# Performance work log

Measured on AMD Instinct MI355X. Metric: run time of the kernel, lower is better.

The kernel has to match this reference:

```python
import jax, jax.numpy as jnp
import numpy as np

B, M, L, IN_C, MID_C, OUT_C = 1, 128, 256, 256, 32, 128


def setup_inputs() -> dict:
    key = jax.random.key(0)
    k_x, k_proj, k_final = jax.random.split(key, 3)
    return {
        "x1d": jax.random.normal(k_x, (B, M, L, IN_C), dtype=jnp.float32),
        "norm_w": jnp.ones((IN_C,), dtype=jnp.float32),
        "norm_b": jnp.zeros((IN_C,), dtype=jnp.float32),
        "proj_w": jax.random.normal(k_proj, (2 * MID_C, IN_C), dtype=jnp.float32) * 0.02,
        "proj_b": jnp.zeros((2 * MID_C,), dtype=jnp.float32),
        "final_w": jax.random.normal(k_final, (OUT_C, MID_C * MID_C), dtype=jnp.float32) * 0.02,
        "final_b": jnp.zeros((OUT_C,), dtype=jnp.float32),
    }


def reference(x1d, norm_w, norm_b, proj_w, proj_b, final_w, final_b):
    # LayerNorm over channel dim
    mu = jnp.mean(x1d, axis=-1, keepdims=True)
    var = jnp.mean(jnp.square(x1d - mu), axis=-1, keepdims=True)
    x = (x1d - mu) * jax.lax.rsqrt(var + 1e-5) * norm_w + norm_b

    mid_c = proj_w.shape[0] // 2
    # Linear -> (b, m, L, 2*mid_c); view (..., mid_c, 2); chunk & squeeze:
    # i = interleaved even channels, j = interleaved odd channels
    p = jnp.einsum('bmlc,dc->bmld', x, proj_w) + proj_b
    p = p.reshape(*p.shape[:-1], mid_c, 2)
    i, j = p[..., 0], p[..., 1]          # each (b, m, L, mid_c)

    m = x1d.shape[1]
    # Outer product mean over the MSA (m) dimension -> (b, L, L, mid_c, mid_c)
    x2d = jnp.einsum('bmix,bmjy->bijxy', i, j) / m

    b, li, lj = x2d.shape[0], x2d.shape[1], x2d.shape[2]
    flat = x2d.reshape(b, li, lj, mid_c * mid_c)
    out = jnp.einsum('bijf,of->bijo', flat, final_w) + final_b
    return out
```

## Files before the change

kernel.cpp:

```cpp
#include <hip/hip_runtime.h>
#include <hip/hip_bf16.h>

#define DEVINL __device__ __forceinline__

typedef float  f32x4_t  __attribute__((ext_vector_type(4)));
typedef float  f32x16_t __attribute__((ext_vector_type(16)));
typedef short  bf16x8_t __attribute__((ext_vector_type(8)));

#define MFMA16(a,b,c) __builtin_amdgcn_mfma_f32_16x16x32_bf16((a),(b),(c),0,0,0)
#define MFMA32(a,b,c) __builtin_amdgcn_mfma_f32_32x32x16_bf16((a),(b),(c),0,0,0)

DEVINL unsigned short f2bf(float f) {
  union { float f; unsigned u; } v; v.f = f;
  unsigned r = v.u + 0x7fffu + ((v.u >> 16) & 1u);
  return (unsigned short)(r >> 16);
}

DEVINL unsigned pk2bf(float lo, float hi) {
  union { __hip_bfloat162 h2; unsigned u; } v;
  v.h2 = __float22bfloat162_rn(make_float2(lo, hi));
  return v.u;
}


__global__ __launch_bounds__(256) void kA(const float* __restrict__ x,
                                          const float* __restrict__ nw,
                                          const float* __restrict__ nb,
                                          const float* __restrict__ pw,
                                          const float* __restrict__ pb,
                                          const float* __restrict__ fw,
                                          unsigned short* __restrict__ Wb,
                                          unsigned short* __restrict__ Ig,
                                          unsigned short* __restrict__ Jg) {
  if (blockIdx.x >= 1024) {
    int T = (blockIdx.x - 1024) * 256 + threadIdx.x;
    int o     = T >> 8;
    int kpos0 = (T & 255) * 4;
    int y  = kpos0 >> 5;
    int x0 = kpos0 & 31;
    const float* fo = fw + o * 1024 + y;
    ushort4 u;
    u.x = f2bf(fo[(x0 + 0) * 32]);
    u.y = f2bf(fo[(x0 + 1) * 32]);
    u.z = f2bf(fo[(x0 + 2) * 32]);
    u.w = f2bf(fo[(x0 + 3) * 32]);
    size_t off = (size_t)((o >> 5) * 64 + (kpos0 >> 4)) * 512 + (o & 31) * 16
               + ((kpos0 >> 3) & 1) * 8 + (kpos0 & 7);
    *(ushort4*)&Wb[off] = u;
    return;
  }
  __shared__ unsigned short xnl[32 * 264];
  __shared__ unsigned short pwl[64 * 264];
  __shared__ unsigned short ep[64 * 36];
  const int tid  = threadIdx.x;
  const int wv   = tid >> 6;
  const int lane = tid & 63;
  const int q    = lane >> 4;
  const int ln16 = lane & 15;
  const int l    = blockIdx.x & 255;
  const int m0   = (blockIdx.x >> 8) * 32;

  const float4* xs = (const float4*)x;
  float4 v[8];
#pragma unroll
  for (int i = 0; i < 8; i++) {
    int row = m0 + i * 4 + wv;
    v[i] = xs[row * 16384 + l * 64 + lane];
  }
  float4 nw4 = ((const float4*)nw)[lane];
  float4 nb4 = ((const float4*)nb)[lane];

#pragma unroll
  for (int i = 0; i < 8; i++) {
    float s  = v[i].x + v[i].y + v[i].z + v[i].w;
    float ss = v[i].x * v[i].x + v[i].y * v[i].y + v[i].z * v[i].z + v[i].w * v[i].w;
#pragma unroll
    for (int off = 32; off > 0; off >>= 1) {
      s  += __shfl_xor(s, off);
      ss += __shfl_xor(ss, off);
    }
    float mu  = s * (1.0f / 256.0f);
    float var = ss * (1.0f / 256.0f) - mu * mu;
    float rs  = rsqrtf(var + 1e-5f);
    ushort4 u;
    u.x = f2bf((v[i].x - mu) * rs * nw4.x + nb4.x);
    u.y = f2bf((v[i].y - mu) * rs * nw4.y + nb4.y);
    u.z = f2bf((v[i].z - mu) * rs * nw4.z + nb4.z);
    u.w = f2bf((v[i].w - mu) * rs * nw4.w + nb4.w);
    *(ushort4*)&xnl[(i * 4 + wv) * 264 + lane * 4] = u;
  }

  const float4* ps = (const float4*)pw;
#pragma unroll
  for (int i = 0; i < 16; i++) {
    float4 w4 = ps[i * 256 + tid];
    ushort4 u;
    u.x = f2bf(w4.x); u.y = f2bf(w4.y); u.z = f2bf(w4.z); u.w = f2bf(w4.w);
    *(ushort4*)&pwl[(i * 4 + wv) * 264 + lane * 4] = u;
  }
  __syncthreads();

  const int rt = wv & 1;
  const int db = (wv >> 1) * 32;
  f32x4_t acc[2] = {{0.f, 0.f, 0.f, 0.f}, {0.f, 0.f, 0.f, 0.f}};
#pragma unroll
  for (int kc = 0; kc < 8; kc++) {
    bf16x8_t a  = *(const bf16x8_t*)&xnl[(rt * 16 + ln16) * 264 + kc * 32 + q * 8];
    bf16x8_t b0 = *(const bf16x8_t*)&pwl[(db + ln16) * 264 + kc * 32 + q * 8];
    bf16x8_t b1 = *(const bf16x8_t*)&pwl[(db + 16 + ln16) * 264 + kc * 32 + q * 8];
    acc[0] = MFMA16(a, b0, acc[0]);
    acc[1] = MFMA16(a, b1, acc[1]);
  }

#pragma unroll
  for (int t2 = 0; t2 < 2; t2++) {
    int d = db + t2 * 16 + ln16;
    float bias  = pb[d];
    float scale = (d & 1) ? 1.0f : (1.0f / 128.0f);
#pragma unroll
    for (int r = 0; r < 4; r++) {
      int mloc = rt * 16 + q * 4 + r;
      ep[d * 36 + mloc] = f2bf((acc[t2][r] + bias) * scale);
    }
  }
  __syncthreads();

  const int h  = tid >> 3;
  const int m4 = tid & 7;
  const size_t off = (size_t)(l * 8 + (m0 >> 4) + (m4 >> 2)) * 512 + h * 16 + ((m4 >> 1) & 1) * 8 + (m4 & 1) * 4;
  ushort4 vi = *(const ushort4*)&ep[(2 * h) * 36 + m4 * 4];
  *(ushort4*)&Ig[off] = vi;
  ushort4 vj = *(const ushort4*)&ep[(2 * h + 1) * 36 + m4 * 4];
  *(ushort4*)&Jg[off] = vj;
}

__global__ __launch_bounds__(256, 2) void kB(const unsigned short* __restrict__ Ig,
                                             const unsigned short* __restrict__ Jg,
                                             const unsigned short* __restrict__ Wb,
                                             const float* __restrict__ fb,
                                             float* __restrict__ out) {
  extern __shared__ unsigned short fl[];
  constexpr int P = 1048;
  const int tid  = threadIdx.x;
  const int w    = tid >> 6;
  const int lane = tid & 63;
  const int ln32 = lane & 31;
  const int h    = lane >> 5;
  const int p    = blockIdx.x >> 4;
  const int t    = blockIdx.x & 15;

  bf16x8_t af[2][8];
#pragma unroll
  for (int u = 0; u < 2; u++)
#pragma unroll
    for (int mc = 0; mc < 8; mc++)
      af[u][mc] = *(const bf16x8_t*)&Ig[(size_t)((p * 2 + u) * 8 + mc) * 512 + ln32 * 16 + h * 8];

#pragma unroll
  for (int s = 0; s < 4; s++) {
    const int jl = 4 * w + s;
    const size_t jbase = (size_t)(t * 16 + jl) * 4096 + ln32 * 16 + h * 8;
    bf16x8_t jb[8];
#pragma unroll
    for (int mc = 0; mc < 8; mc++) jb[mc] = *(const bf16x8_t*)&Jg[jbase + mc * 512];
    f32x16_t c[2];
#pragma unroll
    for (int i = 0; i < 16; i++) { c[0][i] = 0.f; c[1][i] = 0.f; }
#pragma unroll
    for (int mc = 0; mc < 8; mc++) {
      c[0] = MFMA32(af[0][mc], jb[mc], c[0]);
      c[1] = MFMA32(af[1][mc], jb[mc], c[1]);
    }
#pragma unroll
    for (int u = 0; u < 2; u++) {
      unsigned short* fr = &fl[(u * 16 + jl) * P];
#pragma unroll
      for (int g = 0; g < 4; g++) {
        int cp = (4 * ln32 + g) ^ (ln32 & 7);
        uint2 pv;
        pv.x = pk2bf(c[u][4 * g + 0], c[u][4 * g + 1]);
        pv.y = pk2bf(c[u][4 * g + 2], c[u][4 * g + 3]);
        *(uint2*)&fr[cp * 8 + h * 4] = pv;
      }
    }
  }

  const int ot = w;
  const unsigned short* Wp = Wb + (size_t)(ot * 64) * 512 + ln32 * 16 + h * 8;
  bf16x8_t bq[8];
  bq[0] = *(const bf16x8_t*)&Wp[0];
  bq[1] = *(const bf16x8_t*)&Wp[512];

  __syncthreads();

#pragma unroll
  for (int i = 2; i < 8; i++) bq[i] = *(const bf16x8_t*)&Wp[(size_t)i * 512];

#define LDA(kc) (*(const bf16x8_t*)&fl[ln32 * P + \
    (((((kc) * 2 + h)) ^ (((kc) >> 1) & 7)) * 8)])

  f32x16_t o2[2];
#pragma unroll
  for (int i = 0; i < 16; i++) { o2[0][i] = 0.f; o2[1][i] = 0.f; }

  bf16x8_t aq[4];
  aq[0] = LDA(0); aq[1] = LDA(1); aq[2] = LDA(2); aq[3] = LDA(3);

#pragma unroll
  for (int kc = 0; kc < 64; kc += 2) {
    bf16x8_t ac0 = aq[kc & 3],      ac1 = aq[(kc + 1) & 3];
    bf16x8_t bc0 = bq[kc & 7],      bc1 = bq[(kc + 1) & 7];
    if (kc < 60) { aq[kc & 3] = LDA(kc + 4); aq[(kc + 1) & 3] = LDA(kc + 5); }
    if (kc < 56) {
      bq[kc & 7]       = *(const bf16x8_t*)&Wp[(size_t)(kc + 8) * 512];
      bq[(kc + 1) & 7] = *(const bf16x8_t*)&Wp[(size_t)(kc + 9) * 512];
    }
    o2[0] = MFMA32(ac0, bc0, o2[0]);
    o2[1] = MFMA32(ac1, bc1, o2[1]);
  }
#undef LDA

  const float bias = fb[ot * 32 + ln32];
  float* ob = out + ((size_t)(p * 2) * 256 + t * 16) * 128 + ot * 32 + ln32;
#pragma unroll
  for (int r = 0; r < 16; r++) {
    int br = (r & 3) + 8 * (r >> 2) + 4 * h;
    ob[(br >> 4) * 32768 + (br & 15) * 128] = o2[0][r] + o2[1][r] + bias;
  }
}

extern "C" void kernel_launch(void* const* d_in, const int* in_sizes, int n_in,
                              void* d_out, int out_size, void* d_ws, size_t ws_size,
                              hipStream_t stream) {
  const float* x1d     = (const float*)d_in[0];
  const float* norm_w  = (const float*)d_in[1];
  const float* norm_b  = (const float*)d_in[2];
  const float* proj_w  = (const float*)d_in[3];
  const float* proj_b  = (const float*)d_in[4];
  const float* final_w = (const float*)d_in[5];
  const float* final_b = (const float*)d_in[6];
  float* outp          = (float*)d_out;

  unsigned short* Wb  = (unsigned short*)d_ws;
  unsigned short* Igp = Wb + 131072;
  unsigned short* Jgp = Igp + 1048576;

  const int kb_lds = 32 * 1048 * 2;
  hipFuncSetAttribute((const void*)kB, hipFuncAttributeMaxDynamicSharedMemorySize, kb_lds);

  kA<<<1152, 256, 0, stream>>>(x1d, norm_w, norm_b, proj_w, proj_b, final_w, Wb, Igp, Jgp);
  kB<<<2048, 256, kb_lds, stream>>>(Igp, Jgp, Wb, final_b, outp);
}
```

Baseline: 134.8 us.

## Double kB block to 512 threads with split-K final GEMM and LDS reduction

kB now launches 8 waves per block instead of 4. In the first stage each wave computes one of the two outer-product rows, and in the final projection each wave covers half of the K dimension for one output tile. The two K halves are summed through LDS before the bias-add store. This is meant to raise parallelism per block and cut per-wave register pressure, at the cost of an extra barrier and LDS reduction round. Occupancy is still capped by roughly 67KB of LDS per block.

```diff
diff --git a/kernel.cpp b/kernel.cpp
--- a/kernel.cpp
+++ b/kernel.cpp
@@ -134,7 +134,7 @@
   *(ushort4*)&Jg[off] = vj;
 }
 
-__global__ __launch_bounds__(256, 2) void kB(const unsigned short* __restrict__ Ig,
+__global__ __launch_bounds__(512, 4) void kB(const unsigned short* __restrict__ Ig,
                                              const unsigned short* __restrict__ Jg,
                                              const unsigned short* __restrict__ Wb,
                                              const float* __restrict__ fb,
@@ -149,44 +149,39 @@
   const int p    = blockIdx.x >> 4;
   const int t    = blockIdx.x & 15;
 
-  bf16x8_t af[2][8];
-#pragma unroll
-  for (int u = 0; u < 2; u++)
-#pragma unroll
-    for (int mc = 0; mc < 8; mc++)
-      af[u][mc] = *(const bf16x8_t*)&Ig[(size_t)((p * 2 + u) * 8 + mc) * 512 + ln32 * 16 + h * 8];
+  const int u  = w & 1;
+  const int sq = w >> 1;
+  bf16x8_t af[8];
+#pragma unroll
+  for (int mc = 0; mc < 8; mc++)
+    af[mc] = *(const bf16x8_t*)&Ig[(size_t)((p * 2 + u) * 8 + mc) * 512 + ln32 * 16 + h * 8];
 
 #pragma unroll
   for (int s = 0; s < 4; s++) {
-    const int jl = 4 * w + s;
+    const int jl = sq * 4 + s;
     const size_t jbase = (size_t)(t * 16 + jl) * 4096 + ln32 * 16 + h * 8;
     bf16x8_t jb[8];
 #pragma unroll
     for (int mc = 0; mc < 8; mc++) jb[mc] = *(const bf16x8_t*)&Jg[jbase + mc * 512];
-    f32x16_t c[2];
-#pragma unroll
-    for (int i = 0; i < 16; i++) { c[0][i] = 0.f; c[1][i] = 0.f; }
-#pragma unroll
-    for (int mc = 0; mc < 8; mc++) {
-      c[0] = MFMA32(af[0][mc], jb[mc], c[0]);
-      c[1] = MFMA32(af[1][mc], jb[mc], c[1]);
-    }
-#pragma unroll
-    for (int u = 0; u < 2; u++) {
-      unsigned short* fr = &fl[(u * 16 + jl) * P];
-#pragma unroll
-      for (int g = 0; g < 4; g++) {
-        int cp = (4 * ln32 + g) ^ (ln32 & 7);
-        uint2 pv;
-        pv.x = pk2bf(c[u][4 * g + 0], c[u][4 * g + 1]);
-        pv.y = pk2bf(c[u][4 * g + 2], c[u][4 * g + 3]);
-        *(uint2*)&fr[cp * 8 + h * 4] = pv;
-      }
-    }
-  }
-
-  const int ot = w;
-  const unsigned short* Wp = Wb + (size_t)(ot * 64) * 512 + ln32 * 16 + h * 8;
+    f32x16_t c;
+#pragma unroll
+    for (int i = 0; i < 16; i++) c[i] = 0.f;
+#pragma unroll
+    for (int mc = 0; mc < 8; mc++) c = MFMA32(af[mc], jb[mc], c);
+    unsigned short* fr = &fl[(u * 16 + jl) * P];
+#pragma unroll
+    for (int g = 0; g < 4; g++) {
+      int cp = (4 * ln32 + g) ^ (ln32 & 7);
+      uint2 pv;
+      pv.x = pk2bf(c[4 * g + 0], c[4 * g + 1]);
+      pv.y = pk2bf(c[4 * g + 2], c[4 * g + 3]);
+      *(uint2*)&fr[cp * 8 + h * 4] = pv;
+    }
+  }
+
+  const int ot = w & 3;
+  const int kh = w >> 2;
+  const unsigned short* Wp = Wb + (size_t)(ot * 64 + kh * 32) * 512 + ln32 * 16 + h * 8;
   bf16x8_t bq[8];
   bq[0] = *(const bf16x8_t*)&Wp[0];
   bq[1] = *(const bf16x8_t*)&Wp[512];
@@ -197,7 +192,7 @@
   for (int i = 2; i < 8; i++) bq[i] = *(const bf16x8_t*)&Wp[(size_t)i * 512];
 
 #define LDA(kc) (*(const bf16x8_t*)&fl[ln32 * P + \
-    (((((kc) * 2 + h)) ^ (((kc) >> 1) & 7)) * 8)])
+    ((((kh * 32 + (kc)) * 2 + h) ^ (((kh * 32 + (kc)) >> 1) & 7)) * 8)])
 
   f32x16_t o2[2];
 #pragma unroll
@@ -207,11 +202,11 @@
   aq[0] = LDA(0); aq[1] = LDA(1); aq[2] = LDA(2); aq[3] = LDA(3);
 
 #pragma unroll
-  for (int kc = 0; kc < 64; kc += 2) {
+  for (int kc = 0; kc < 32; kc += 2) {
     bf16x8_t ac0 = aq[kc & 3],      ac1 = aq[(kc + 1) & 3];
     bf16x8_t bc0 = bq[kc & 7],      bc1 = bq[(kc + 1) & 7];
-    if (kc < 60) { aq[kc & 3] = LDA(kc + 4); aq[(kc + 1) & 3] = LDA(kc + 5); }
-    if (kc < 56) {
+    if (kc < 28) { aq[kc & 3] = LDA(kc + 4); aq[(kc + 1) & 3] = LDA(kc + 5); }
+    if (kc < 24) {
       bq[kc & 7]       = *(const bf16x8_t*)&Wp[(size_t)(kc + 8) * 512];
       bq[(kc + 1) & 7] = *(const bf16x8_t*)&Wp[(size_t)(kc + 9) * 512];
     }
@@ -220,12 +215,35 @@
   }
 #undef LDA
 
-  const float bias = fb[ot * 32 + ln32];
-  float* ob = out + ((size_t)(p * 2) * 256 + t * 16) * 128 + ot * 32 + ln32;
-#pragma unroll
-  for (int r = 0; r < 16; r++) {
-    int br = (r & 3) + 8 * (r >> 2) + 4 * h;
-    ob[(br >> 4) * 32768 + (br & 15) * 128] = o2[0][r] + o2[1][r] + bias;
+#pragma unroll
+  for (int i = 0; i < 16; i++) o2[0][i] += o2[1][i];
+
+  __syncthreads();
+  float* red = (float*)fl;
+  if (kh == 1) {
+#pragma unroll
+    for (int q = 0; q < 4; q++) {
+      int idx = ot * 1024 + lane * 16 + ((q ^ (lane & 3)) * 4);
+      *(float4*)&red[idx] = make_float4(o2[0][4 * q + 0], o2[0][4 * q + 1],
+                                        o2[0][4 * q + 2], o2[0][4 * q + 3]);
+    }
+  }
+  __syncthreads();
+  if (kh == 0) {
+#pragma unroll
+    for (int q = 0; q < 4; q++) {
+      int idx = ot * 1024 + lane * 16 + ((q ^ (lane & 3)) * 4);
+      float4 rv = *(const float4*)&red[idx];
+      o2[0][4 * q + 0] += rv.x; o2[0][4 * q + 1] += rv.y;
+      o2[0][4 * q + 2] += rv.z; o2[0][4 * q + 3] += rv.w;
+    }
+    const float bias = fb[ot * 32 + ln32];
+    float* ob = out + ((size_t)(p * 2) * 256 + t * 16) * 128 + ot * 32 + ln32;
+#pragma unroll
+    for (int r = 0; r < 16; r++) {
+      int br = (r & 3) + 8 * (r >> 2) + 4 * h;
+      ob[(br >> 4) * 32768 + (br & 15) * 128] = o2[0][r] + bias;
+    }
   }
 }
 
@@ -249,5 +267,5 @@
   hipFuncSetAttribute((const void*)kB, hipFuncAttributeMaxDynamicSharedMemorySize, kb_lds);
 
   kA<<<1152, 256, 0, stream>>>(x1d, norm_w, norm_b, proj_w, proj_b, final_w, Wb, Igp, Jgp);
-  kB<<<2048, 256, kb_lds, stream>>>(Igp, Jgp, Wb, final_b, outp);
-}
+  kB<<<2048, 512, kb_lds, stream>>>(Igp, Jgp, Wb, final_b, outp);
+}
```

New measurement: 138.8 us. 3.0% more time.

## Process all 128 MSA rows per block in kA to amortize proj weight loads

Applied to the files above, without the earlier changes.

kA now launches one 512-thread block per sequence position l, covering all 128 m rows instead of 32, so proj_w is converted to bf16 and staged in LDS once per l rather than four times. The final_w bf16 repacking is folded into the first 128 threads of each block instead of using separate extra blocks. The LDS row padding changes from 264 to 268 and LDS becomes dynamic. In exchange the grid shrinks from 1152 to 256 blocks, which is about one block per CU, and each thread holds 16 float4 registers, so there is less parallelism to hide memory latency.

```diff
diff --git a/kernel.cpp b/kernel.cpp
--- a/kernel.cpp
+++ b/kernel.cpp
@@ -23,7 +23,7 @@
 }
 
 
-__global__ __launch_bounds__(256) void kA(const float* __restrict__ x,
+__global__ __launch_bounds__(512) void kA(const float* __restrict__ x,
                                           const float* __restrict__ nw,
                                           const float* __restrict__ nb,
                                           const float* __restrict__ pw,
@@ -32,8 +32,27 @@
                                           unsigned short* __restrict__ Wb,
                                           unsigned short* __restrict__ Ig,
                                           unsigned short* __restrict__ Jg) {
-  if (blockIdx.x >= 1024) {
-    int T = (blockIdx.x - 1024) * 256 + threadIdx.x;
+  extern __shared__ unsigned short sA[];
+  unsigned short* xnl = sA;
+  unsigned short* pwl = sA + 128 * 268;
+  unsigned short* ep  = sA + (128 + 64) * 268;
+  const int tid  = threadIdx.x;
+  const int wv   = tid >> 6;
+  const int lane = tid & 63;
+  const int q    = lane >> 4;
+  const int ln16 = lane & 15;
+  const int l    = blockIdx.x;
+
+  const float4* xs = (const float4*)x;
+  float4 v[16];
+#pragma unroll
+  for (int i = 0; i < 16; i++)
+    v[i] = xs[(size_t)(i * 8 + wv) * 16384 + l * 64 + lane];
+  float4 nw4 = ((const float4*)nw)[lane];
+  float4 nb4 = ((const float4*)nb)[lane];
+
+  if (tid < 128) {
+    int T = blockIdx.x * 128 + tid;
     int o     = T >> 8;
     int kpos0 = (T & 255) * 4;
     int y  = kpos0 >> 5;
@@ -47,31 +66,22 @@
     size_t off = (size_t)((o >> 5) * 64 + (kpos0 >> 4)) * 512 + (o & 31) * 16
                + ((kpos0 >> 3) & 1) * 8 + (kpos0 & 7);
     *(ushort4*)&Wb[off] = u;
-    return;
-  }
-  __shared__ unsigned short xnl[32 * 264];
-  __shared__ unsigned short pwl[64 * 264];
-  __shared__ unsigned short ep[64 * 36];
-  const int tid  = threadIdx.x;
-  const int wv   = tid >> 6;
-  const int lane = tid & 63;
-  const int q    = lane >> 4;
-  const int ln16 = lane & 15;
-  const int l    = blockIdx.x & 255;
-  const int m0   = (blockIdx.x >> 8) * 32;
-
-  const float4* xs = (const float4*)x;
-  float4 v[8];
+  }
+
+  const float4* ps = (const float4*)pw;
 #pragma unroll
   for (int i = 0; i < 8; i++) {
-    int row = m0 + i * 4 + wv;
-    v[i] = xs[row * 16384 + l * 64 + lane];
-  }
-  float4 nw4 = ((const float4*)nw)[lane];
-  float4 nb4 = ((const float4*)nb)[lane];
-
-#pragma unroll
-  for (int i = 0; i < 8; i++) {
+    int idx  = i * 512 + tid;
+    int row  = idx >> 6;
+    int col4 = idx & 63;
+    float4 w4 = ps[idx];
+    ushort4 u;
+    u.x = f2bf(w4.x); u.y = f2bf(w4.y); u.z = f2bf(w4.z); u.w = f2bf(w4.w);
+    *(ushort4*)&pwl[row * 268 + col4 * 4] = u;
+  }
+
+#pragma unroll
+  for (int i = 0; i < 16; i++) {
     float s  = v[i].x + v[i].y + v[i].z + v[i].w;
     float ss = v[i].x * v[i].x + v[i].y * v[i].y + v[i].z * v[i].z + v[i].w * v[i].w;
 #pragma unroll
@@ -87,51 +97,43 @@
     u.y = f2bf((v[i].y - mu) * rs * nw4.y + nb4.y);
     u.z = f2bf((v[i].z - mu) * rs * nw4.z + nb4.z);
     u.w = f2bf((v[i].w - mu) * rs * nw4.w + nb4.w);
-    *(ushort4*)&xnl[(i * 4 + wv) * 264 + lane * 4] = u;
-  }
-
-  const float4* ps = (const float4*)pw;
-#pragma unroll
-  for (int i = 0; i < 16; i++) {
-    float4 w4 = ps[i * 256 + tid];
-    ushort4 u;
-    u.x = f2bf(w4.x); u.y = f2bf(w4.y); u.z = f2bf(w4.z); u.w = f2bf(w4.w);
-    *(ushort4*)&pwl[(i * 4 + wv) * 264 + lane * 4] = u;
+    *(ushort4*)&xnl[(i * 8 + wv) * 268 + lane * 4] = u;
   }
   __syncthreads();
 
-  const int rt = wv & 1;
-  const int db = (wv >> 1) * 32;
-  f32x4_t acc[2] = {{0.f, 0.f, 0.f, 0.f}, {0.f, 0.f, 0.f, 0.f}};
+  f32x4_t acc[4] = {{0,0,0,0},{0,0,0,0},{0,0,0,0},{0,0,0,0}};
 #pragma unroll
   for (int kc = 0; kc < 8; kc++) {
-    bf16x8_t a  = *(const bf16x8_t*)&xnl[(rt * 16 + ln16) * 264 + kc * 32 + q * 8];
-    bf16x8_t b0 = *(const bf16x8_t*)&pwl[(db + ln16) * 264 + kc * 32 + q * 8];
-    bf16x8_t b1 = *(const bf16x8_t*)&pwl[(db + 16 + ln16) * 264 + kc * 32 + q * 8];
-    acc[0] = MFMA16(a, b0, acc[0]);
-    acc[1] = MFMA16(a, b1, acc[1]);
-  }
-
-#pragma unroll
-  for (int t2 = 0; t2 < 2; t2++) {
-    int d = db + t2 * 16 + ln16;
+    bf16x8_t a = *(const bf16x8_t*)&xnl[(wv * 16 + ln16) * 268 + kc * 32 + q * 8];
+#pragma unroll
+    for (int dt = 0; dt < 4; dt++) {
+      bf16x8_t b = *(const bf16x8_t*)&pwl[(dt * 16 + ln16) * 268 + kc * 32 + q * 8];
+      acc[dt] = MFMA16(a, b, acc[dt]);
+    }
+  }
+#pragma unroll
+  for (int dt = 0; dt < 4; dt++) {
+    int d = dt * 16 + ln16;
     float bias  = pb[d];
     float scale = (d & 1) ? 1.0f : (1.0f / 128.0f);
 #pragma unroll
-    for (int r = 0; r < 4; r++) {
-      int mloc = rt * 16 + q * 4 + r;
-      ep[d * 36 + mloc] = f2bf((acc[t2][r] + bias) * scale);
-    }
+    for (int r = 0; r < 4; r++)
+      ep[d * 132 + wv * 16 + q * 4 + r] = f2bf((acc[dt][r] + bias) * scale);
   }
   __syncthreads();
 
-  const int h  = tid >> 3;
-  const int m4 = tid & 7;
-  const size_t off = (size_t)(l * 8 + (m0 >> 4) + (m4 >> 2)) * 512 + h * 16 + ((m4 >> 1) & 1) * 8 + (m4 & 1) * 4;
-  ushort4 vi = *(const ushort4*)&ep[(2 * h) * 36 + m4 * 4];
-  *(ushort4*)&Ig[off] = vi;
-  ushort4 vj = *(const ushort4*)&ep[(2 * h + 1) * 36 + m4 * 4];
-  *(ushort4*)&Jg[off] = vj;
+  const int hh  = tid >> 4;
+  const int mg0 = tid & 15;
+#pragma unroll
+  for (int g2 = 0; g2 < 2; g2++) {
+    int mg = g2 * 16 + mg0;
+    size_t off = (size_t)(l * 8 + (mg >> 2)) * 512 + hh * 16
+               + ((mg >> 1) & 1) * 8 + (mg & 1) * 4;
+    ushort4 vi = *(const ushort4*)&ep[(2 * hh) * 132 + mg * 4];
+    *(ushort4*)&Ig[off] = vi;
+    ushort4 vj = *(const ushort4*)&ep[(2 * hh + 1) * 132 + mg * 4];
+    *(ushort4*)&Jg[off] = vj;
+  }
 }
 
 __global__ __launch_bounds__(256, 2) void kB(const unsigned short* __restrict__ Ig,
@@ -245,9 +247,11 @@
   unsigned short* Igp = Wb + 131072;
   unsigned short* Jgp = Igp + 1048576;
 
+  const int ka_lds = (128 * 268 + 64 * 268 + 64 * 132) * 2;
   const int kb_lds = 32 * 1048 * 2;
+  hipFuncSetAttribute((const void*)kA, hipFuncAttributeMaxDynamicSharedMemorySize, ka_lds);
   hipFuncSetAttribute((const void*)kB, hipFuncAttributeMaxDynamicSharedMemorySize, kb_lds);
 
-  kA<<<1152, 256, 0, stream>>>(x1d, norm_w, norm_b, proj_w, proj_b, final_w, Wb, Igp, Jgp);
+  kA<<<256, 512, ka_lds, stream>>>(x1d, norm_w, norm_b, proj_w, proj_b, final_w, Wb, Igp, Jgp);
   kB<<<2048, 256, kb_lds, stream>>>(Igp, Jgp, Wb, final_b, outp);
 }
```

Measured after the change: 148.4 us. 10.1% more time.

## Split final GEMM over K across waves with LDS reduction; fold weight conversion into kA

Applied to the files above, without the earlier changes.

In kB, each wave now takes a quarter of the K dimension and computes all four output tiles, instead of each wave owning one output tile over the full K. This lets one A fragment feed four MFMAs. Partial sums are reduced through LDS by wave 0, and s_setprio is wrapped around the MFMA bursts. In kA, the final_w bf16 conversion moves into the first 128 normal blocks, so the 128 extra blocks go away. The change adds an LDS reduction, two extra barriers and a serial epilogue on wave 0.

```diff
diff --git a/kernel.cpp b/kernel.cpp
--- a/kernel.cpp
+++ b/kernel.cpp
@@ -32,8 +32,29 @@
                                           unsigned short* __restrict__ Wb,
                                           unsigned short* __restrict__ Ig,
                                           unsigned short* __restrict__ Jg) {
-  if (blockIdx.x >= 1024) {
-    int T = (blockIdx.x - 1024) * 256 + threadIdx.x;
+  __shared__ unsigned short xnl[32 * 264];
+  __shared__ unsigned short pwl[64 * 264];
+  __shared__ unsigned short ep[64 * 36];
+  const int tid  = threadIdx.x;
+  const int wv   = tid >> 6;
+  const int lane = tid & 63;
+  const int q    = lane >> 4;
+  const int ln16 = lane & 15;
+  const int l    = blockIdx.x & 255;
+  const int m0   = (blockIdx.x >> 8) * 32;
+
+  const float4* xs = (const float4*)x;
+  float4 v[8];
+#pragma unroll
+  for (int i = 0; i < 8; i++) {
+    int row = m0 + i * 4 + wv;
+    v[i] = xs[row * 16384 + l * 64 + lane];
+  }
+  float4 nw4 = ((const float4*)nw)[lane];
+  float4 nb4 = ((const float4*)nb)[lane];
+
+  if (blockIdx.x < 128) {
+    int T = blockIdx.x * 256 + tid;
     int o     = T >> 8;
     int kpos0 = (T & 255) * 4;
     int y  = kpos0 >> 5;
@@ -47,28 +68,7 @@
     size_t off = (size_t)((o >> 5) * 64 + (kpos0 >> 4)) * 512 + (o & 31) * 16
                + ((kpos0 >> 3) & 1) * 8 + (kpos0 & 7);
     *(ushort4*)&Wb[off] = u;
-    return;
-  }
-  __shared__ unsigned short xnl[32 * 264];
-  __shared__ unsigned short pwl[64 * 264];
-  __shared__ unsigned short ep[64 * 36];
-  const int tid  = threadIdx.x;
-  const int wv   = tid >> 6;
-  const int lane = tid & 63;
-  const int q    = lane >> 4;
-  const int ln16 = lane & 15;
-  const int l    = blockIdx.x & 255;
-  const int m0   = (blockIdx.x >> 8) * 32;
-
-  const float4* xs = (const float4*)x;
-  float4 v[8];
-#pragma unroll
-  for (int i = 0; i < 8; i++) {
-    int row = m0 + i * 4 + wv;
-    v[i] = xs[row * 16384 + l * 64 + lane];
-  }
-  float4 nw4 = ((const float4*)nw)[lane];
-  float4 nb4 = ((const float4*)nb)[lane];
+  }
 
 #pragma unroll
   for (int i = 0; i < 8; i++) {
@@ -185,47 +185,89 @@
     }
   }
 
-  const int ot = w;
-  const unsigned short* Wp = Wb + (size_t)(ot * 64) * 512 + ln32 * 16 + h * 8;
-  bf16x8_t bq[8];
-  bq[0] = *(const bf16x8_t*)&Wp[0];
-  bq[1] = *(const bf16x8_t*)&Wp[512];
-
-  __syncthreads();
-
-#pragma unroll
-  for (int i = 2; i < 8; i++) bq[i] = *(const bf16x8_t*)&Wp[(size_t)i * 512];
+  const int kq = w;
+  const unsigned short* WpK = Wb + (size_t)(kq * 16) * 512 + ln32 * 16 + h * 8;
+  bf16x8_t bq[4][4];
+#pragma unroll
+  for (int ot = 0; ot < 4; ot++)
+    bq[0][ot] = *(const bf16x8_t*)&WpK[(size_t)(ot * 64) * 512];
+
+  __syncthreads();
+
+#pragma unroll
+  for (int kc2 = 1; kc2 < 4; kc2++)
+#pragma unroll
+    for (int ot = 0; ot < 4; ot++)
+      bq[kc2][ot] = *(const bf16x8_t*)&WpK[(size_t)(ot * 64 + kc2) * 512];
 
 #define LDA(kc) (*(const bf16x8_t*)&fl[ln32 * P + \
-    (((((kc) * 2 + h)) ^ (((kc) >> 1) & 7)) * 8)])
-
-  f32x16_t o2[2];
-#pragma unroll
-  for (int i = 0; i < 16; i++) { o2[0][i] = 0.f; o2[1][i] = 0.f; }
+    ((((kq * 16 + (kc)) * 2 + h) ^ (((kq * 16 + (kc)) >> 1) & 7)) * 8)])
+
+  f32x16_t oa[4];
+#pragma unroll
+  for (int ot = 0; ot < 4; ot++)
+#pragma unroll
+    for (int i = 0; i < 16; i++) oa[ot][i] = 0.f;
 
   bf16x8_t aq[4];
   aq[0] = LDA(0); aq[1] = LDA(1); aq[2] = LDA(2); aq[3] = LDA(3);
 
 #pragma unroll
-  for (int kc = 0; kc < 64; kc += 2) {
-    bf16x8_t ac0 = aq[kc & 3],      ac1 = aq[(kc + 1) & 3];
-    bf16x8_t bc0 = bq[kc & 7],      bc1 = bq[(kc + 1) & 7];
-    if (kc < 60) { aq[kc & 3] = LDA(kc + 4); aq[(kc + 1) & 3] = LDA(kc + 5); }
-    if (kc < 56) {
-      bq[kc & 7]       = *(const bf16x8_t*)&Wp[(size_t)(kc + 8) * 512];
-      bq[(kc + 1) & 7] = *(const bf16x8_t*)&Wp[(size_t)(kc + 9) * 512];
-    }
-    o2[0] = MFMA32(ac0, bc0, o2[0]);
-    o2[1] = MFMA32(ac1, bc1, o2[1]);
+  for (int kc = 0; kc < 16; kc++) {
+    bf16x8_t ac = aq[kc & 3];
+    bf16x8_t b0 = bq[kc & 3][0], b1 = bq[kc & 3][1];
+    bf16x8_t b2 = bq[kc & 3][2], b3 = bq[kc & 3][3];
+    if (kc < 12) {
+      aq[kc & 3] = LDA(kc + 4);
+#pragma unroll
+      for (int ot = 0; ot < 4; ot++)
+        bq[kc & 3][ot] = *(const bf16x8_t*)&WpK[(size_t)(ot * 64 + kc + 4) * 512];
+    }
+    __builtin_amdgcn_s_setprio(1);
+    oa[0] = MFMA32(ac, b0, oa[0]);
+    oa[1] = MFMA32(ac, b1, oa[1]);
+    oa[2] = MFMA32(ac, b2, oa[2]);
+    oa[3] = MFMA32(ac, b3, oa[3]);
+    __builtin_amdgcn_s_setprio(0);
   }
 #undef LDA
 
-  const float bias = fb[ot * 32 + ln32];
-  float* ob = out + ((size_t)(p * 2) * 256 + t * 16) * 128 + ot * 32 + ln32;
-#pragma unroll
-  for (int r = 0; r < 16; r++) {
-    int br = (r & 3) + 8 * (r >> 2) + 4 * h;
-    ob[(br >> 4) * 32768 + (br & 15) * 128] = o2[0][r] + o2[1][r] + bias;
+  __syncthreads();
+  float* red = (float*)fl;
+  if (kq != 0) {
+#pragma unroll
+    for (int ot = 0; ot < 4; ot++) {
+      float* bb = red + ((kq - 1) * 4 + ot) * 1092 + lane * 17;
+#pragma unroll
+      for (int g = 0; g < 4; g++)
+        *(float4*)&bb[g * 4] = make_float4(oa[ot][4 * g + 0], oa[ot][4 * g + 1],
+                                           oa[ot][4 * g + 2], oa[ot][4 * g + 3]);
+    }
+  }
+  __syncthreads();
+  if (kq == 0) {
+#pragma unroll
+    for (int s3 = 0; s3 < 3; s3++)
+#pragma unroll
+      for (int ot = 0; ot < 4; ot++) {
+        const float* bb = red + (s3 * 4 + ot) * 1092 + lane * 17;
+#pragma unroll
+        for (int g = 0; g < 4; g++) {
+          float4 rv = *(const float4*)&bb[g * 4];
+          oa[ot][4 * g + 0] += rv.x; oa[ot][4 * g + 1] += rv.y;
+          oa[ot][4 * g + 2] += rv.z; oa[ot][4 * g + 3] += rv.w;
+        }
+      }
+#pragma unroll
+    for (int ot = 0; ot < 4; ot++) {
+      const float bias = fb[ot * 32 + ln32];
+      float* ob = out + ((size_t)(p * 2) * 256 + t * 16) * 128 + ot * 32 + ln32;
+#pragma unroll
+      for (int r = 0; r < 16; r++) {
+        int br = (r & 3) + 8 * (r >> 2) + 4 * h;
+        ob[(br >> 4) * 32768 + (br & 15) * 128] = oa[ot][r] + bias;
+      }
+    }
   }
 }
 
@@ -248,6 +290,6 @@
   const int kb_lds = 32 * 1048 * 2;
   hipFuncSetAttribute((const void*)kB, hipFuncAttributeMaxDynamicSharedMemorySize, kb_lds);
 
-  kA<<<1152, 256, 0, stream>>>(x1d, norm_w, norm_b, proj_w, proj_b, final_w, Wb, Igp, Jgp);
+  kA<<<1024, 256, 0, stream>>>(x1d, norm_w, norm_b, proj_w, proj_b, final_w, Wb, Igp, Jgp);
   kB<<<2048, 256, kb_lds, stream>>>(Igp, Jgp, Wb, final_b, outp);
 }
```

Result: slower. 148.8 us (+10.4%).
